# Kernel optimization log

Hardware: AMD Instinct MI355X
Metric: run time of the kernel (lower is better)

Reference implementation:

```python
import jax, jax.numpy as jnp
import numpy as np

N_NODES = 50000
N_EDGES = 800000
N_IN = 256
N_H = 64


def _xavier(key, fan_in, fan_out):
    limit = np.sqrt(6.0 / (fan_in + fan_out)).astype(np.float32)
    return jax.random.uniform(key, (fan_in, fan_out), jnp.float32, -limit, limit)


def setup_inputs() -> dict:
    key = jax.random.key(0)
    ks = jax.random.split(key, 12)
    inp = {
        "bf": jax.random.normal(ks[0], (1, N_NODES, N_IN), jnp.float32),
        "bl": jax.random.normal(ks[1], (1, N_NODES, N_IN), jnp.float32),
        "shuf_fts": jax.random.normal(ks[2], (1, N_NODES, N_IN), jnp.float32),
        "shuf_fls": jax.random.normal(ks[3], (1, N_NODES, N_IN), jnp.float32),
        "adj_rows": jax.random.randint(ks[4], (N_EDGES,), 0, N_NODES, jnp.int32),
        "adj_cols": jax.random.randint(ks[5], (N_EDGES,), 0, N_NODES, jnp.int32),
        "adj_w": jax.random.uniform(ks[6], (N_EDGES,), jnp.float32),
        "diff_rows": jax.random.randint(ks[7], (N_EDGES,), 0, N_NODES, jnp.int32),
        "diff_cols": jax.random.randint(ks[8], (N_EDGES,), 0, N_NODES, jnp.int32),
        "diff_w": jax.random.uniform(ks[9], (N_EDGES,), jnp.float32),
        # GCN parameters (Linear has bias=False; separate additive bias init 0; PReLU slope 0.25)
        "W1": _xavier(ks[10], N_IN, N_H),
        "b1": jnp.zeros((N_H,), jnp.float32),
        "a1": jnp.float32(0.25),
        "W2": _xavier(ks[11], N_IN, N_H),
        "b2": jnp.zeros((N_H,), jnp.float32),
        "a2": jnp.float32(0.25),
    }
    return inp


def _gcn(seq, W, b, a, rows, cols, w):
    # seq: [1, N, F_in]; sparse spmm: out[r] = sum_e 1[rows[e]==r] * w[e] * fts[cols[e]]
    fts = seq[0] @ W                                   # [N, n_h]
    msgs = w[:, None] * fts[cols]                      # [E, n_h] gather
    agg = jax.ops.segment_sum(msgs, rows, num_segments=N_NODES)  # [N, n_h] scatter-add
    out = agg[None, :, :] + b                          # bias add
    return jnp.where(out >= 0, out, a * out)           # PReLU


def reference(bf, bl, shuf_fts, shuf_fls, adj_rows, adj_cols, adj_w,
              diff_rows, diff_cols, diff_w, W1, b1, a1, W2, b2, a2):
    h_1 = _gcn(bf, W1, b1, a1, adj_rows, adj_cols, adj_w)
    h_2 = _gcn(bl, W2, b2, a2, diff_rows, diff_cols, diff_w)
    h_3 = _gcn(shuf_fts, W1, b1, a1, adj_rows, adj_cols, adj_w)
    h_4 = _gcn(shuf_fls, W2, b2, a2, diff_rows, diff_cols, diff_w)
    return jnp.stack([h_1, h_2, h_3, h_4])             # [4, 1, N, n_h]
```

## Files before the change

kernel.cpp:

```cpp
#include <hip/hip_runtime.h>
#include <hip/hip_bf16.h>

#define N_NODES 50000
#define N_EDGES 800000
#define N_IN    256
#define N_H     64
#define NB      125
#define RPB     400
#define BCAP    8192
#define EPT     8
#define BIN_BLK 2048
#define GSTRIDE 256
#define ASTRIDE 264

typedef short short8 __attribute__((ext_vector_type(8)));
typedef float f32x4  __attribute__((ext_vector_type(4)));

__device__ inline short f2bf(float f) {
    __bf16 h = (__bf16)f;
    return (short)__builtin_bit_cast(unsigned short, h);
}
__device__ inline float bflo(unsigned int q) { return __uint_as_float(q << 16); }
__device__ inline float bfhi(unsigned int q) { return __uint_as_float(q & 0xFFFF0000u); }


__global__ __launch_bounds__(256) void k_bin(
    const int* __restrict__ adj_rows, const int* __restrict__ adj_cols,
    const float* __restrict__ adj_w,
    const int* __restrict__ diff_rows, const int* __restrict__ diff_cols,
    const float* __restrict__ diff_w,
    int* __restrict__ gcnt, int2* __restrict__ bin) {

    int g = blockIdx.y;
    const int*   rows = g ? diff_rows : adj_rows;
    const int*   cols = g ? diff_cols : adj_cols;
    const float* ww   = g ? diff_w    : adj_w;
    int base_e = blockIdx.x * BIN_BLK;
    int t = threadIdx.x;

    __shared__ int lcnt[NB];
    __shared__ int lbase[NB];
    for (int i = t; i < NB; i += 256) lcnt[i] = 0;
    __syncthreads();

    int lpos[EPT];
    int bkt[EPT];
    #pragma unroll
    for (int e = 0; e < EPT; ++e) {
        int idx = base_e + e * 256 + t;
        if (idx < N_EDGES) {
            int r = rows[idx];
            int b = r / RPB;
            bkt[e] = b;
            lpos[e] = atomicAdd(&lcnt[b], 1);
        } else bkt[e] = -1;
    }
    __syncthreads();
    for (int i = t; i < NB; i += 256) lbase[i] = atomicAdd(&gcnt[g * NB + i], lcnt[i]);
    __syncthreads();

    #pragma unroll
    for (int e = 0; e < EPT; ++e) {
        int idx = base_e + e * 256 + t;
        if (idx < N_EDGES) {
            unsigned int r = (unsigned int)rows[idx];
            unsigned int c = (unsigned int)cols[idx];
            int b = bkt[e];
            int2 m;
            m.x = (int)((r << 16) | c);
            m.y = __float_as_int(ww[idx]);
            bin[((size_t)(g * NB + b)) * BCAP + lbase[b] + lpos[e]] = m;
        }
    }
}


__global__ __launch_bounds__(256) void k_build(
    const int* __restrict__ gcnt, const int2* __restrict__ bin,
    int2* __restrict__ csr, int* __restrict__ row_ptr) {

    int g = blockIdx.y, b = blockIdx.x, t = threadIdx.x;
    __shared__ int hist[512];
    __shared__ int s2[256];
    __shared__ int sbase;

    for (int i = t; i < 512; i += 256) hist[i] = 0;
    __syncthreads();

    int cnt = gcnt[g * NB + b];
    const int2* be = bin + ((size_t)(g * NB + b)) * BCAP;
    int r0 = b * RPB;

    for (int i = t; i < cnt; i += 256) {
        unsigned int rc = (unsigned int)be[i].x;
        atomicAdd(&hist[(rc >> 16) - r0], 1);
    }
    __syncthreads();

    if (t == 0) {
        int s = 0;
        for (int i = 0; i < b; ++i) s += gcnt[g * NB + i];
        sbase = s;
    }

    int v0 = hist[2 * t], v1 = hist[2 * t + 1];
    int local = v0 + v1;
    s2[t] = local;
    __syncthreads();
    for (int off = 1; off < 256; off <<= 1) {
        int v = (t >= off) ? s2[t - off] : 0;
        __syncthreads();
        s2[t] += v;
        __syncthreads();
    }
    int e0 = sbase + (s2[t] - local);
    int e1 = e0 + v0;

    int* rp = row_ptr + g * (N_NODES + 1);
    if (2 * t < RPB)     rp[r0 + 2 * t]     = e0;
    if (2 * t + 1 < RPB) rp[r0 + 2 * t + 1] = e1;
    __syncthreads();
    hist[2 * t] = e0;
    hist[2 * t + 1] = e1;
    __syncthreads();

    int2* cg = csr + (size_t)g * N_EDGES;
    for (int i = t; i < cnt; i += 256) {
        int2 m = be[i];
        unsigned int rc = (unsigned int)m.x;
        int lr = (int)(rc >> 16) - r0;
        int pos = atomicAdd(&hist[lr], 1);
        int2 o;
        o.x = (int)(rc & 0xFFFFu);
        o.y = m.y;
        cg[pos] = o;
    }
    if (b == NB - 1 && t == 0) rp[N_NODES] = N_EDGES;
}


__global__ __launch_bounds__(256) void k_wt(const float* __restrict__ W1,
                                            const float* __restrict__ W2,
                                            unsigned short* __restrict__ WTg) {
    int g = blockIdx.x;
    const float* W = g ? W2 : W1;
    unsigned short* o = WTg + (size_t)g * 64 * GSTRIDE;
    for (int i = threadIdx.x; i < N_IN * N_H; i += 256) {
        int k = i >> 6, c = i & 63;
        o[c * GSTRIDE + k] = (unsigned short)f2bf(W[i]);
    }
}


__global__ __launch_bounds__(256, 4) void k_gemm(
    const float* __restrict__ X0, const float* __restrict__ X1,
    const float* __restrict__ X2, const float* __restrict__ X3,
    const unsigned short* __restrict__ WTg,
    unsigned short* __restrict__ Tadj, unsigned short* __restrict__ Tdiff) {

    int gy = blockIdx.y;
    int g = gy >> 1, s = gy & 1;
    const float* X = g ? (s ? X3 : X1) : (s ? X2 : X0);
    unsigned short* T = g ? Tdiff : Tadj;
    const unsigned short* WB = WTg + (size_t)g * 64 * GSTRIDE;
    int coloff = s * 64;

    int t    = threadIdx.x;
    int wid  = t >> 6;
    int lane = t & 63;
    int l15  = lane & 15;
    int kg   = lane >> 4;
    int rb0  = blockIdx.x * 32;

    __shared__ __align__(16) unsigned short A[32 * ASTRIDE];

    float4 v[4];
    #pragma unroll
    for (int j = 0; j < 4; ++j) {
        int idx = t + 256 * j;
        int row = idx >> 6, col4 = idx & 63;
        int grow = rb0 + row; if (grow >= N_NODES) grow = N_NODES - 1;
        v[j] = ((const float4*)(X + (size_t)grow * N_IN))[col4];
    }

    int ctbase = (wid >> 1) * 2;
    short8 bfr[2][8];
    #pragma unroll
    for (int c2 = 0; c2 < 2; ++c2) {
        int ct = ctbase + c2;
        #pragma unroll
        for (int kt = 0; kt < 8; ++kt) {
            bfr[c2][kt] = *reinterpret_cast<const short8*>(
                WB + ((ct * 16 + l15) * GSTRIDE + kt * 32 + kg * 8));
        }
    }

    #pragma unroll
    for (int j = 0; j < 4; ++j) {
        int idx = t + 256 * j;
        int row = idx >> 6, col4 = idx & 63;
        ushort4 c;
        c.x = (unsigned short)f2bf(v[j].x);
        c.y = (unsigned short)f2bf(v[j].y);
        c.z = (unsigned short)f2bf(v[j].z);
        c.w = (unsigned short)f2bf(v[j].w);
        *reinterpret_cast<ushort4*>(&A[row * ASTRIDE + col4 * 4]) = c;
    }
    #pragma unroll
    for (int j = 4; j < 8; ++j) {
        int idx = t + 256 * j;
        int row = idx >> 6, col4 = idx & 63;
        int grow = rb0 + row; if (grow >= N_NODES) grow = N_NODES - 1;
        v[j - 4] = ((const float4*)(X + (size_t)grow * N_IN))[col4];
    }
    #pragma unroll
    for (int j = 4; j < 8; ++j) {
        int idx = t + 256 * j;
        int row = idx >> 6, col4 = idx & 63;
        ushort4 c;
        c.x = (unsigned short)f2bf(v[j - 4].x);
        c.y = (unsigned short)f2bf(v[j - 4].y);
        c.z = (unsigned short)f2bf(v[j - 4].z);
        c.w = (unsigned short)f2bf(v[j - 4].w);
        *reinterpret_cast<ushort4*>(&A[row * ASTRIDE + col4 * 4]) = c;
    }
    __syncthreads();

    int rt = wid & 1;
    f32x4 acc[2];
    acc[0] = (f32x4){0.f, 0.f, 0.f, 0.f};
    acc[1] = (f32x4){0.f, 0.f, 0.f, 0.f};

    #pragma unroll
    for (int kt = 0; kt < 8; ++kt) {
        short8 af = *reinterpret_cast<const short8*>(
            &A[(rt * 16 + l15) * ASTRIDE + kt * 32 + kg * 8]);
        acc[0] = __builtin_amdgcn_mfma_f32_16x16x32_bf16(af, bfr[0][kt], acc[0], 0, 0, 0);
        acc[1] = __builtin_amdgcn_mfma_f32_16x16x32_bf16(af, bfr[1][kt], acc[1], 0, 0, 0);
    }

    #pragma unroll
    for (int c2 = 0; c2 < 2; ++c2) {
        int col = coloff + (ctbase + c2) * 16 + l15;
        #pragma unroll
        for (int r = 0; r < 4; ++r) {
            int row = rb0 + rt * 16 + kg * 4 + r;
            if (row < N_NODES)
                T[(size_t)row * 128 + col] = (unsigned short)f2bf(acc[c2][r]);
        }
    }
}


__global__ __launch_bounds__(256) void k_agg(
    const int* __restrict__ row_ptr, const int2* __restrict__ csr,
    const unsigned int* __restrict__ Tadj, const unsigned int* __restrict__ Tdiff,
    const float* __restrict__ b1, const float* __restrict__ a1,
    const float* __restrict__ b2, const float* __restrict__ a2,
    float* __restrict__ out) {

    int wid  = threadIdx.x >> 6;
    int lane = threadIdx.x & 63;
    int node = blockIdx.x * 4 + wid;
    int g    = blockIdx.y;

    const int* rp = row_ptr + g * (N_NODES + 1);
    const int2* el = csr + (size_t)g * N_EDGES;
    const unsigned int* Tu = g ? Tdiff : Tadj;

    int e  = rp[node];
    int e1 = rp[node + 1];
    float ax = 0.f, ay = 0.f;

    for (; e + 4 <= e1; e += 4) {
        int2 m0 = el[e + 0], m1 = el[e + 1], m2 = el[e + 2], m3 = el[e + 3];
        unsigned int q0 = Tu[(size_t)m0.x * 64 + lane];
        unsigned int q1 = Tu[(size_t)m1.x * 64 + lane];
        unsigned int q2 = Tu[(size_t)m2.x * 64 + lane];
        unsigned int q3 = Tu[(size_t)m3.x * 64 + lane];
        float w0 = __int_as_float(m0.y), w1 = __int_as_float(m1.y);
        float w2 = __int_as_float(m2.y), w3 = __int_as_float(m3.y);
        ax += w0 * bflo(q0); ay += w0 * bfhi(q0);
        ax += w1 * bflo(q1); ay += w1 * bfhi(q1);
        ax += w2 * bflo(q2); ay += w2 * bfhi(q2);
        ax += w3 * bflo(q3); ay += w3 * bfhi(q3);
    }
    for (; e < e1; ++e) {
        int2 m = el[e];
        unsigned int q = Tu[(size_t)m.x * 64 + lane];
        float w = __int_as_float(m.y);
        ax += w * bflo(q); ay += w * bfhi(q);
    }

    const float* bias = g ? b2 : b1;
    float slope = g ? a2[0] : a1[0];
    int f = 2 * lane;
    size_t base;
    int fo;
    if (lane < 32) { base = g ? (size_t)3200000 : (size_t)0;       fo = f; }
    else           { base = g ? (size_t)9600000 : (size_t)6400000; fo = f - 64; }
    float v0 = ax + bias[fo];
    float v1 = ay + bias[fo + 1];
    v0 = (v0 >= 0.f) ? v0 : slope * v0;
    v1 = (v1 >= 0.f) ? v1 : slope * v1;
    float2 res; res.x = v0; res.y = v1;
    *reinterpret_cast<float2*>(out + base + (size_t)node * 64 + fo) = res;
}


extern "C" void kernel_launch(void* const* d_in, const int* in_sizes, int n_in,
                              void* d_out, int out_size, void* d_ws, size_t ws_size,
                              hipStream_t stream) {
    const float* bf_      = (const float*)d_in[0];
    const float* bl_      = (const float*)d_in[1];
    const float* shuf_fts = (const float*)d_in[2];
    const float* shuf_fls = (const float*)d_in[3];
    const int*   adj_rows = (const int*)d_in[4];
    const int*   adj_cols = (const int*)d_in[5];
    const float* adj_w    = (const float*)d_in[6];
    const int*   diff_rows= (const int*)d_in[7];
    const int*   diff_cols= (const int*)d_in[8];
    const float* diff_w   = (const float*)d_in[9];
    const float* W1       = (const float*)d_in[10];
    const float* b1       = (const float*)d_in[11];
    const float* a1       = (const float*)d_in[12];
    const float* W2       = (const float*)d_in[13];
    const float* b2       = (const float*)d_in[14];
    const float* a2       = (const float*)d_in[15];
    float* out = (float*)d_out;

    char* ws = (char*)d_ws;
    unsigned short* Tadj  = (unsigned short*)(ws);
    unsigned short* Tdiff = (unsigned short*)(ws + 12800000);
    int2* csr             = (int2*)(ws + 25600000);
    int*  row_ptr         = (int*)(ws + 38400000);
    int*  gcnt            = (int*)(ws + 38801024);
    unsigned short* WTg   = (unsigned short*)(ws + 38803072);

    int2* bin = (int2*)d_out;

    hipMemsetAsync(gcnt, 0, 2 * NB * sizeof(int), stream);

    k_bin<<<dim3((N_EDGES + BIN_BLK - 1) / BIN_BLK, 2), dim3(256), 0, stream>>>(
        adj_rows, adj_cols, adj_w, diff_rows, diff_cols, diff_w, gcnt, bin);
    k_wt<<<dim3(2), dim3(256), 0, stream>>>(W1, W2, WTg);
    k_build<<<dim3(NB, 2), dim3(256), 0, stream>>>(gcnt, bin, csr, row_ptr);

    k_gemm<<<dim3((N_NODES + 31) / 32, 4), dim3(256), 0, stream>>>(
        bf_, bl_, shuf_fts, shuf_fls, WTg, Tadj, Tdiff);

    k_agg<<<dim3(N_NODES / 4, 2), dim3(256), 0, stream>>>(
        row_ptr, csr, (const unsigned int*)Tadj, (const unsigned int*)Tdiff,
        b1, a1, b2, a2, out);
}
```

Baseline: 225.6 us.

## Make GEMM persistent with register double-buffered prefetch of next tile

Result: faster. 206.4 us (-8.5%).

```diff
diff --git a/kernel.cpp b/kernel.cpp
--- a/kernel.cpp
+++ b/kernel.cpp
@@ -12,6 +12,8 @@
 #define BIN_BLK 2048
 #define GSTRIDE 256
 #define ASTRIDE 264
+#define NTILES  1563
+#define GEMMX   192
 
 typedef short short8 __attribute__((ext_vector_type(8)));
 typedef float f32x4  __attribute__((ext_vector_type(4)));
@@ -152,7 +154,7 @@
 }
 
 
-__global__ __launch_bounds__(256, 4) void k_gemm(
+__global__ __launch_bounds__(256, 3) void k_gemm(
     const float* __restrict__ X0, const float* __restrict__ X1,
     const float* __restrict__ X2, const float* __restrict__ X3,
     const unsigned short* __restrict__ WTg,
@@ -170,18 +172,9 @@
     int lane = t & 63;
     int l15  = lane & 15;
     int kg   = lane >> 4;
-    int rb0  = blockIdx.x * 32;
+    int col4 = t & 63;
 
     __shared__ __align__(16) unsigned short A[32 * ASTRIDE];
-
-    float4 v[4];
-    #pragma unroll
-    for (int j = 0; j < 4; ++j) {
-        int idx = t + 256 * j;
-        int row = idx >> 6, col4 = idx & 63;
-        int grow = rb0 + row; if (grow >= N_NODES) grow = N_NODES - 1;
-        v[j] = ((const float4*)(X + (size_t)grow * N_IN))[col4];
-    }
 
     int ctbase = (wid >> 1) * 2;
     short8 bfr[2][8];
@@ -195,59 +188,70 @@
         }
     }
 
-    #pragma unroll
-    for (int j = 0; j < 4; ++j) {
-        int idx = t + 256 * j;
-        int row = idx >> 6, col4 = idx & 63;
-        ushort4 c;
-        c.x = (unsigned short)f2bf(v[j].x);
-        c.y = (unsigned short)f2bf(v[j].y);
-        c.z = (unsigned short)f2bf(v[j].z);
-        c.w = (unsigned short)f2bf(v[j].w);
-        *reinterpret_cast<ushort4*>(&A[row * ASTRIDE + col4 * 4]) = c;
-    }
-    #pragma unroll
-    for (int j = 4; j < 8; ++j) {
-        int idx = t + 256 * j;
-        int row = idx >> 6, col4 = idx & 63;
-        int grow = rb0 + row; if (grow >= N_NODES) grow = N_NODES - 1;
-        v[j - 4] = ((const float4*)(X + (size_t)grow * N_IN))[col4];
-    }
-    #pragma unroll
-    for (int j = 4; j < 8; ++j) {
-        int idx = t + 256 * j;
-        int row = idx >> 6, col4 = idx & 63;
-        ushort4 c;
-        c.x = (unsigned short)f2bf(v[j - 4].x);
-        c.y = (unsigned short)f2bf(v[j - 4].y);
-        c.z = (unsigned short)f2bf(v[j - 4].z);
-        c.w = (unsigned short)f2bf(v[j - 4].w);
-        *reinterpret_cast<ushort4*>(&A[row * ASTRIDE + col4 * 4]) = c;
-    }
-    __syncthreads();
-
     int rt = wid & 1;
-    f32x4 acc[2];
-    acc[0] = (f32x4){0.f, 0.f, 0.f, 0.f};
-    acc[1] = (f32x4){0.f, 0.f, 0.f, 0.f};
-
-    #pragma unroll
-    for (int kt = 0; kt < 8; ++kt) {
-        short8 af = *reinterpret_cast<const short8*>(
-            &A[(rt * 16 + l15) * ASTRIDE + kt * 32 + kg * 8]);
-        acc[0] = __builtin_amdgcn_mfma_f32_16x16x32_bf16(af, bfr[0][kt], acc[0], 0, 0, 0);
-        acc[1] = __builtin_amdgcn_mfma_f32_16x16x32_bf16(af, bfr[1][kt], acc[1], 0, 0, 0);
-    }
-
-    #pragma unroll
-    for (int c2 = 0; c2 < 2; ++c2) {
-        int col = coloff + (ctbase + c2) * 16 + l15;
-        #pragma unroll
-        for (int r = 0; r < 4; ++r) {
-            int row = rb0 + rt * 16 + kg * 4 + r;
-            if (row < N_NODES)
-                T[(size_t)row * 128 + col] = (unsigned short)f2bf(acc[c2][r]);
-        }
+    int tile = blockIdx.x;
+
+    float4 v[8], v2[8];
+    {
+        int base = tile * 32 + wid;
+        #pragma unroll
+        for (int j = 0; j < 8; ++j) {
+            int grow = base + 4 * j; if (grow >= N_NODES) grow = N_NODES - 1;
+            v[j] = ((const float4*)(X + (size_t)grow * N_IN))[col4];
+        }
+    }
+
+    while (tile < NTILES) {
+        int nxt = tile + GEMMX;
+        if (nxt < NTILES) {
+            int base = nxt * 32 + wid;
+            #pragma unroll
+            for (int j = 0; j < 8; ++j) {
+                int grow = base + 4 * j; if (grow >= N_NODES) grow = N_NODES - 1;
+                v2[j] = ((const float4*)(X + (size_t)grow * N_IN))[col4];
+            }
+        }
+        __builtin_amdgcn_sched_barrier(0);
+
+        #pragma unroll
+        for (int j = 0; j < 8; ++j) {
+            int row = wid + 4 * j;
+            ushort4 c;
+            c.x = (unsigned short)f2bf(v[j].x);
+            c.y = (unsigned short)f2bf(v[j].y);
+            c.z = (unsigned short)f2bf(v[j].z);
+            c.w = (unsigned short)f2bf(v[j].w);
+            *reinterpret_cast<ushort4*>(&A[row * ASTRIDE + col4 * 4]) = c;
+        }
+        __syncthreads();
+
+        f32x4 acc[2];
+        acc[0] = (f32x4){0.f, 0.f, 0.f, 0.f};
+        acc[1] = (f32x4){0.f, 0.f, 0.f, 0.f};
+        #pragma unroll
+        for (int kt = 0; kt < 8; ++kt) {
+            short8 af = *reinterpret_cast<const short8*>(
+                &A[(rt * 16 + l15) * ASTRIDE + kt * 32 + kg * 8]);
+            acc[0] = __builtin_amdgcn_mfma_f32_16x16x32_bf16(af, bfr[0][kt], acc[0], 0, 0, 0);
+            acc[1] = __builtin_amdgcn_mfma_f32_16x16x32_bf16(af, bfr[1][kt], acc[1], 0, 0, 0);
+        }
+
+        int rb0 = tile * 32;
+        #pragma unroll
+        for (int c2 = 0; c2 < 2; ++c2) {
+            int col = coloff + (ctbase + c2) * 16 + l15;
+            #pragma unroll
+            for (int r = 0; r < 4; ++r) {
+                int row = rb0 + rt * 16 + kg * 4 + r;
+                if (row < N_NODES)
+                    T[(size_t)row * 128 + col] = (unsigned short)f2bf(acc[c2][r]);
+            }
+        }
+        __syncthreads();
+
+        tile = nxt;
+        #pragma unroll
+        for (int j = 0; j < 8; ++j) v[j] = v2[j];
     }
 }
 
@@ -346,7 +350,7 @@
     k_wt<<<dim3(2), dim3(256), 0, stream>>>(W1, W2, WTg);
     k_build<<<dim3(NB, 2), dim3(256), 0, stream>>>(gcnt, bin, csr, row_ptr);
 
-    k_gemm<<<dim3((N_NODES + 31) / 32, 4), dim3(256), 0, stream>>>(
+    k_gemm<<<dim3(GEMMX, 4), dim3(256), 0, stream>>>(
         bf_, bl_, shuf_fts, shuf_fls, WTg, Tadj, Tdiff);
 
     k_agg<<<dim3(N_NODES / 4, 2), dim3(256), 0, stream>>>(
```
